# Kernel tuning notes

Measured on AMD Instinct MI355X. Metric: run time of the kernel, lower is better.

Reference implementation:

```python
import jax, jax.numpy as jnp
import numpy as np

D, N_EXP, TOP_K = 2048, 64, 8
B, S = 4, 4096

def setup_inputs() -> dict:
    key = jax.random.key(0)
    k1, k2, k3, k4 = jax.random.split(key, 4)
    hidden_states = jax.random.normal(k1, (B, S, D), dtype=jnp.float32)
    # nn.Linear weights are [out, in]; default init ~ U(-1/sqrt(d), 1/sqrt(d))
    bound = 1.0 / np.sqrt(D)
    W_gate = jax.random.uniform(k2, (N_EXP, D), jnp.float32, -bound, bound)
    W_noise = 0.01 * jax.random.normal(k3, (N_EXP, D), dtype=jnp.float32)
    # training-mode noise (router_step % top_k == 0 path): fixed-seed randn
    noise = jax.random.normal(k4, (B, S, N_EXP), dtype=jnp.float32)
    return {"hidden_states": hidden_states, "W_gate": W_gate,
            "W_noise": W_noise, "noise": noise}

def reference(hidden_states, W_gate, W_noise, noise):
    # logits = h @ W_gate^T  : [B,S,n_exp]
    logits = jnp.einsum('bsd,ed->bse', hidden_states, W_gate)
    scale = jax.nn.softplus(jnp.einsum('bsd,ed->bse', hidden_states, W_noise))
    logits = logits + noise * scale
    gates = jax.nn.softmax(logits, axis=-1)
    vals, inds = jax.lax.top_k(gates, TOP_K)  # sorted desc (torch used sorted=False)
    return vals, inds, gates
```

## Files before the change

kernel.cpp:

```cpp
#include <hip/hip_runtime.h>
#include <math.h>

typedef __attribute__((ext_vector_type(8)))  _Float16 half8;
typedef __attribute__((ext_vector_type(4)))  float    f32x4;
typedef __attribute__((ext_vector_type(16))) float    f32x16;

constexpr int D_DIM = 2048;
constexpr int NEXP  = 64;
constexpr int TOPK  = 8;
constexpr int NTOK  = 16384;
constexpr int TM    = 64;
constexpr int BK    = 64;
constexpr int NCH   = D_DIM / BK;
constexpr int OSTR  = 132;
constexpr float WSCALE  = 4096.0f;
constexpr float INV_WSC = 1.0f / 4096.0f;

__device__ __forceinline__ unsigned short f16b(float x) {
    _Float16 h = (_Float16)x;
    return __builtin_bit_cast(unsigned short, h);
}
__device__ __forceinline__ float f16tof(unsigned short b) {
    return (float)__builtin_bit_cast(_Float16, b);
}
__device__ __forceinline__ f32x4 ntload4(const float* p) {
    return __builtin_nontemporal_load(reinterpret_cast<const f32x4*>(p));
}

__global__ void prep_w(const float* __restrict__ Wg, const float* __restrict__ Wn,
                       unsigned short* __restrict__ wsB)
{
    const int idx = blockIdx.x * blockDim.x + threadIdx.x;
    const int n   = idx >> 8;
    const int K8  = idx & 255;
    const float* src = (n < 64) ? (Wg + (size_t)n * D_DIM)
                                : (Wn + (size_t)(n - 64) * D_DIM);
    f32x4 a = *reinterpret_cast<const f32x4*>(src + K8 * 8);
    f32x4 b = *reinterpret_cast<const f32x4*>(src + K8 * 8 + 4);

    float v[8] = {a[0], a[1], a[2], a[3], b[0], b[1], b[2], b[3]};
    union { unsigned short u[8]; half8 s; } H, L;
#pragma unroll
    for (int j = 0; j < 8; ++j) {
        float xs = v[j] * WSCALE;
        unsigned short h = f16b(xs);
        H.u[j] = h;
        L.u[j] = f16b(xs - f16tof(h));
    }
    const int kk   = K8 >> 1;
    const int koct = K8 & 1;
    const int lane = koct * 32 + (n & 31);
    const size_t base = (size_t)kk * 4096 + (size_t)(n >> 5) * 1024 + (size_t)lane * 8;
    *reinterpret_cast<half8*>(wsB + base)       = H.s;
    *reinterpret_cast<half8*>(wsB + base + 512) = L.s;
}

__global__ __launch_bounds__(512, 2)
void noisy_topk_router(const float* __restrict__ hs,
                       const unsigned short* __restrict__ wsB,
                       const float* __restrict__ nz,
                       float* __restrict__ out)
{
    __shared__ __align__(16) char smem[33792];
    unsigned short* stage  = reinterpret_cast<unsigned short*>(smem);
    float*          logits = reinterpret_cast<float*>(smem);

    const int tid  = threadIdx.x;
    const int lane = tid & 63;
    const int w    = tid >> 6;
    const int mt   = w & 1;
    const int nt   = w >> 1;
    const int t0   = blockIdx.x * TM;

    const int lxr = lane ^ ((lane >> 5) << 2);

    const int r    = tid >> 3;
    const int q    = tid & 7;
    const int ks_w = q >> 1;
    const int koct = q & 1;
    const int uphys = ((koct << 5) + (r & 31)) ^ ks_w ^ (koct << 2);
    const int woff  = (ks_w * 2 + (r >> 5)) * 1024 + uphys * 8;
    const float* hrow = hs + (size_t)(t0 + r) * D_DIM + q * 8;

    const unsigned short* bbase = wsB + (size_t)nt * 1024 + (size_t)lane * 8;

    f32x16 accP, accX0, accX1;
#pragma unroll
    for (int i = 0; i < 16; ++i) { accP[i] = 0.f; accX0[i] = 0.f; accX1[i] = 0.f; }

    half8 bh0[4], bl0[4], bh1[4], bl1[4];

    auto loadB = [&](int chunk, half8* bh, half8* bl) {
#pragma unroll
        for (int ks = 0; ks < 4; ++ks) {
            const unsigned short* p = bbase + (size_t)(chunk * 4 + ks) * 4096;
            bh[ks] = *reinterpret_cast<const half8*>(p);
            bl[ks] = *reinterpret_cast<const half8*>(p + 512);
        }
    };

    auto cvt_write = [&](f32x4 a, f32x4 b, unsigned short* buf) {
        float v[8] = {a[0], a[1], a[2], a[3], b[0], b[1], b[2], b[3]};
        union { unsigned short u[8]; half8 s; } H, L;
#pragma unroll
        for (int j = 0; j < 8; ++j) {
            unsigned short h = f16b(v[j]);
            H.u[j] = h;
            L.u[j] = f16b(v[j] - f16tof(h));
        }
        *reinterpret_cast<half8*>(buf + woff)       = H.s;
        *reinterpret_cast<half8*>(buf + woff + 512) = L.s;
    };

    auto body = [&](const half8* bh, const half8* bl, const unsigned short* sb) {
#pragma unroll
        for (int ks = 0; ks < 4; ++ks) {
            const int off = (ks * 2 + mt) * 1024 + (lxr ^ ks) * 8;
            half8 ahi = *reinterpret_cast<const half8*>(sb + off);
            half8 alo = *reinterpret_cast<const half8*>(sb + off + 512);
            accP  = __builtin_amdgcn_mfma_f32_32x32x16_f16(ahi, bh[ks], accP,  0, 0, 0);
            accX0 = __builtin_amdgcn_mfma_f32_32x32x16_f16(ahi, bl[ks], accX0, 0, 0, 0);
            accX1 = __builtin_amdgcn_mfma_f32_32x32x16_f16(alo, bh[ks], accX1, 0, 0, 0);
        }
    };

    loadB(0, bh0, bl0);
    cvt_write(ntload4(hrow), ntload4(hrow + 4), stage);
    __syncthreads();

#pragma unroll 1
    for (int cc = 0; cc < NCH / 2; ++cc) {
        const int e = 2 * cc;
        loadB(e + 1, bh1, bl1);
        __builtin_amdgcn_sched_barrier(0);
        f32x4 pa = ntload4(hrow + (e + 1) * BK);
        f32x4 pb = ntload4(hrow + (e + 1) * BK + 4);
        __builtin_amdgcn_sched_barrier(0);
        body(bh0, bl0, stage);
        cvt_write(pa, pb, stage + 8192);
        __syncthreads();

        const bool more = (e + 2) < NCH;
        f32x4 pa2, pb2;
        if (more) {
            loadB(e + 2, bh0, bl0);
            __builtin_amdgcn_sched_barrier(0);
            pa2 = ntload4(hrow + (e + 2) * BK);
            pb2 = ntload4(hrow + (e + 2) * BK + 4);
            __builtin_amdgcn_sched_barrier(0);
        }
        body(bh1, bl1, stage + 8192);
        if (more)
            cvt_write(pa2, pb2, stage);
        __syncthreads();
    }

    {
        const int colb  = nt * 32 + (lane & 31);
        const int rbase = mt * 32 + 4 * (lane >> 5);
#pragma unroll
        for (int rr = 0; rr < 16; ++rr) {
            const int row = rbase + (rr & 3) + 8 * (rr >> 2);
            logits[row * OSTR + colb] = (accP[rr] + accX0[rr] + accX1[rr]) * INV_WSC;
        }
    }
    __syncthreads();

    float* gout = out + (size_t)NTOK * TOPK * 2;
    for (int tt = 0; tt < 8; ++tt) {
        const int tl  = w * 8 + tt;
        const int tok = t0 + tl;
        float gsc = logits[tl * OSTR + lane];
        float nl  = logits[tl * OSTR + 64 + lane];
        float nzv = __builtin_nontemporal_load(nz + (size_t)tok * NEXP + lane);
        float sp  = fmaxf(nl, 0.0f) + log1pf(expf(-fabsf(nl)));
        float le  = fmaf(nzv, sp, gsc);

        float mx = le;
#pragma unroll
        for (int d = 32; d > 0; d >>= 1) mx = fmaxf(mx, __shfl_xor(mx, d));
        float pe = expf(le - mx);
        float s  = pe;
#pragma unroll
        for (int d = 32; d > 0; d >>= 1) s += __shfl_xor(s, d);
        float g = pe * (1.0f / s);

        gout[(size_t)tok * NEXP + lane] = g;

        float v = g;
        float keepv = 0.0f;
        int   keepi = 0;
#pragma unroll
        for (int it = 0; it < TOPK; ++it) {
            float m  = v;
            int   mi = lane;
#pragma unroll
            for (int d = 32; d > 0; d >>= 1) {
                float om = __shfl_xor(m, d);
                int   oi = __shfl_xor(mi, d);
                bool take = (om > m) || (om == m && oi < mi);
                m  = take ? om : m;
                mi = take ? oi : mi;
            }
            if (lane == it) { keepv = m; keepi = mi; }
            if (lane == mi) v = -1.0f;
        }
        if (lane < TOPK) {
            out[(size_t)tok * TOPK + lane] = keepv;
            out[(size_t)NTOK * TOPK + (size_t)tok * TOPK + lane] = (float)keepi;
        }
    }
}

extern "C" void kernel_launch(void* const* d_in, const int* in_sizes, int n_in,
                              void* d_out, int out_size, void* d_ws, size_t ws_size,
                              hipStream_t stream) {
    const float* hs = (const float*)d_in[0];
    const float* Wg = (const float*)d_in[1];
    const float* Wn = (const float*)d_in[2];
    const float* nz = (const float*)d_in[3];
    float* out = (float*)d_out;
    unsigned short* wsB = (unsigned short*)d_ws;

    prep_w<<<64, 512, 0, stream>>>(Wg, Wn, wsB);
    noisy_topk_router<<<NTOK / TM, 512, 0, stream>>>(hs, wsB, nz, out);
}
```

Baseline: 254.5 us.

## Load activations straight into MFMA registers and drop LDS staging

Removes the shared-memory staging of the fp32 hidden-state tile. Each wave now loads its 32 token rows directly from global memory into registers and does the fp16 hi/lo split in-register right before the MFMAs. The block shrinks to 32 tokens and 4 waves, each owning 32 of the 128 output columns, and weight loads become nontemporal. This cuts LDS writes and reads plus the block-wide syncs per chunk. In exchange, every wave reloads and reconverts the same A rows, which means 4x redundant global/L1 traffic and VALU conversion work.

```diff
diff --git a/kernel.cpp b/kernel.cpp
--- a/kernel.cpp
+++ b/kernel.cpp
@@ -1,17 +1,17 @@
 #include <hip/hip_runtime.h>
 #include <math.h>
 
-typedef __attribute__((ext_vector_type(8)))  _Float16 half8;
-typedef __attribute__((ext_vector_type(4)))  float    f32x4;
-typedef __attribute__((ext_vector_type(16))) float    f32x16;
+typedef __attribute__((ext_vector_type(8)))  _Float16       half8;
+typedef __attribute__((ext_vector_type(8)))  unsigned short ushort8;
+typedef __attribute__((ext_vector_type(4)))  float          f32x4;
+typedef __attribute__((ext_vector_type(16))) float          f32x16;
 
 constexpr int D_DIM = 2048;
 constexpr int NEXP  = 64;
 constexpr int TOPK  = 8;
 constexpr int NTOK  = 16384;
-constexpr int TM    = 64;
-constexpr int BK    = 64;
-constexpr int NCH   = D_DIM / BK;
+constexpr int TM    = 32;
+constexpr int NCH   = 32;
 constexpr int OSTR  = 132;
 constexpr float WSCALE  = 4096.0f;
 constexpr float INV_WSC = 1.0f / 4096.0f;
@@ -23,8 +23,9 @@
 __device__ __forceinline__ float f16tof(unsigned short b) {
     return (float)__builtin_bit_cast(_Float16, b);
 }
-__device__ __forceinline__ f32x4 ntload4(const float* p) {
-    return __builtin_nontemporal_load(reinterpret_cast<const f32x4*>(p));
+__device__ __forceinline__ half8 ntloadB(const unsigned short* p) {
+    ushort8 u = __builtin_nontemporal_load(reinterpret_cast<const ushort8*>(p));
+    return __builtin_bit_cast(half8, u);
 }
 
 __global__ void prep_w(const float* __restrict__ Wg, const float* __restrict__ Wn,
@@ -55,109 +56,86 @@
     *reinterpret_cast<half8*>(wsB + base + 512) = L.s;
 }
 
-__global__ __launch_bounds__(512, 2)
+__global__ __launch_bounds__(256, 2)
 void noisy_topk_router(const float* __restrict__ hs,
                        const unsigned short* __restrict__ wsB,
                        const float* __restrict__ nz,
                        float* __restrict__ out)
 {
-    __shared__ __align__(16) char smem[33792];
-    unsigned short* stage  = reinterpret_cast<unsigned short*>(smem);
-    float*          logits = reinterpret_cast<float*>(smem);
+    __shared__ __align__(16) float logits[TM * OSTR];
 
     const int tid  = threadIdx.x;
     const int lane = tid & 63;
     const int w    = tid >> 6;
-    const int mt   = w & 1;
-    const int nt   = w >> 1;
+    const int nt   = w;
     const int t0   = blockIdx.x * TM;
 
-    const int lxr = lane ^ ((lane >> 5) << 2);
-
-    const int r    = tid >> 3;
-    const int q    = tid & 7;
-    const int ks_w = q >> 1;
-    const int koct = q & 1;
-    const int uphys = ((koct << 5) + (r & 31)) ^ ks_w ^ (koct << 2);
-    const int woff  = (ks_w * 2 + (r >> 5)) * 1024 + uphys * 8;
-    const float* hrow = hs + (size_t)(t0 + r) * D_DIM + q * 8;
-
+    const int mrow = lane & 31;
+    const int koct = lane >> 5;
+    const float* abase = hs + (size_t)(t0 + mrow) * D_DIM + koct * 8;
     const unsigned short* bbase = wsB + (size_t)nt * 1024 + (size_t)lane * 8;
 
     f32x16 accP, accX0, accX1;
 #pragma unroll
     for (int i = 0; i < 16; ++i) { accP[i] = 0.f; accX0[i] = 0.f; accX1[i] = 0.f; }
 
+    f32x4 A0[4][2], A1[4][2];
     half8 bh0[4], bl0[4], bh1[4], bl1[4];
 
+    auto loadA = [&](int chunk, f32x4 (*A)[2]) {
+#pragma unroll
+        for (int ks = 0; ks < 4; ++ks) {
+            const float* p = abase + (size_t)(chunk * 4 + ks) * 16;
+            A[ks][0] = *reinterpret_cast<const f32x4*>(p);
+            A[ks][1] = *reinterpret_cast<const f32x4*>(p + 4);
+        }
+    };
     auto loadB = [&](int chunk, half8* bh, half8* bl) {
 #pragma unroll
         for (int ks = 0; ks < 4; ++ks) {
             const unsigned short* p = bbase + (size_t)(chunk * 4 + ks) * 4096;
-            bh[ks] = *reinterpret_cast<const half8*>(p);
-            bl[ks] = *reinterpret_cast<const half8*>(p + 512);
+            bh[ks] = ntloadB(p);
+            bl[ks] = ntloadB(p + 512);
         }
     };
-
-    auto cvt_write = [&](f32x4 a, f32x4 b, unsigned short* buf) {
-        float v[8] = {a[0], a[1], a[2], a[3], b[0], b[1], b[2], b[3]};
-        union { unsigned short u[8]; half8 s; } H, L;
-#pragma unroll
-        for (int j = 0; j < 8; ++j) {
-            unsigned short h = f16b(v[j]);
-            H.u[j] = h;
-            L.u[j] = f16b(v[j] - f16tof(h));
-        }
-        *reinterpret_cast<half8*>(buf + woff)       = H.s;
-        *reinterpret_cast<half8*>(buf + woff + 512) = L.s;
+    auto body = [&](f32x4 (*A)[2], const half8* bh, const half8* bl) {
+#pragma unroll
+        for (int ks = 0; ks < 4; ++ks) {
+            float v[8] = {A[ks][0][0], A[ks][0][1], A[ks][0][2], A[ks][0][3],
+                          A[ks][1][0], A[ks][1][1], A[ks][1][2], A[ks][1][3]};
+            union { unsigned short u[8]; half8 s; } H, L;
+#pragma unroll
+            for (int j = 0; j < 8; ++j) {
+                unsigned short h = f16b(v[j]);
+                H.u[j] = h;
+                L.u[j] = f16b(v[j] - f16tof(h));
+            }
+            accP  = __builtin_amdgcn_mfma_f32_32x32x16_f16(H.s, bh[ks], accP,  0, 0, 0);
+            accX0 = __builtin_amdgcn_mfma_f32_32x32x16_f16(H.s, bl[ks], accX0, 0, 0, 0);
+            accX1 = __builtin_amdgcn_mfma_f32_32x32x16_f16(L.s, bh[ks], accX1, 0, 0, 0);
+        }
     };
 
-    auto body = [&](const half8* bh, const half8* bl, const unsigned short* sb) {
-#pragma unroll
-        for (int ks = 0; ks < 4; ++ks) {
-            const int off = (ks * 2 + mt) * 1024 + (lxr ^ ks) * 8;
-            half8 ahi = *reinterpret_cast<const half8*>(sb + off);
-            half8 alo = *reinterpret_cast<const half8*>(sb + off + 512);
-            accP  = __builtin_amdgcn_mfma_f32_32x32x16_f16(ahi, bh[ks], accP,  0, 0, 0);
-            accX0 = __builtin_amdgcn_mfma_f32_32x32x16_f16(ahi, bl[ks], accX0, 0, 0, 0);
-            accX1 = __builtin_amdgcn_mfma_f32_32x32x16_f16(alo, bh[ks], accX1, 0, 0, 0);
-        }
-    };
-
+    loadA(0, A0);
     loadB(0, bh0, bl0);
-    cvt_write(ntload4(hrow), ntload4(hrow + 4), stage);
-    __syncthreads();
 
 #pragma unroll 1
     for (int cc = 0; cc < NCH / 2; ++cc) {
         const int e = 2 * cc;
+        loadA(e + 1, A1);
         loadB(e + 1, bh1, bl1);
-        __builtin_amdgcn_sched_barrier(0);
-        f32x4 pa = ntload4(hrow + (e + 1) * BK);
-        f32x4 pb = ntload4(hrow + (e + 1) * BK + 4);
-        __builtin_amdgcn_sched_barrier(0);
-        body(bh0, bl0, stage);
-        cvt_write(pa, pb, stage + 8192);
-        __syncthreads();
-
-        const bool more = (e + 2) < NCH;
-        f32x4 pa2, pb2;
-        if (more) {
+        body(A0, bh0, bl0);
+        if (e + 2 < NCH) {
+            loadA(e + 2, A0);
             loadB(e + 2, bh0, bl0);
-            __builtin_amdgcn_sched_barrier(0);
-            pa2 = ntload4(hrow + (e + 2) * BK);
-            pb2 = ntload4(hrow + (e + 2) * BK + 4);
-            __builtin_amdgcn_sched_barrier(0);
-        }
-        body(bh1, bl1, stage + 8192);
-        if (more)
-            cvt_write(pa2, pb2, stage);
-        __syncthreads();
+        }
+        body(A1, bh1, bl1);
+        __builtin_amdgcn_s_barrier();
     }
 
     {
         const int colb  = nt * 32 + (lane & 31);
-        const int rbase = mt * 32 + 4 * (lane >> 5);
+        const int rbase = 4 * (lane >> 5);
 #pragma unroll
         for (int rr = 0; rr < 16; ++rr) {
             const int row = rbase + (rr & 3) + 8 * (rr >> 2);
@@ -223,5 +201,5 @@
     unsigned short* wsB = (unsigned short*)d_ws;
 
     prep_w<<<64, 512, 0, stream>>>(Wg, Wn, wsB);
-    noisy_topk_router<<<NTOK / TM, 512, 0, stream>>>(hs, wsB, nz, out);
-}
+    noisy_topk_router<<<NTOK / TM, 256, 0, stream>>>(hs, wsB, nz, out);
+}
```

New measurement: 294.8 us. 15.8% more time.
